# Kernel tuning notes

Hardware: AMD Instinct MI355X
Metric: run time of the kernel (lower is better)

Reference implementation:

```python
import jax, jax.numpy as jnp
import numpy as np

B, L, C, D, M = 64, 256, 8, 512, 512


def setup_inputs() -> dict:
    key = jax.random.key(0)
    ks = jax.random.split(key, 12)
    sd = 1.0 / np.sqrt(D)
    sm = 1.0 / np.sqrt(M)
    return {
        "x": jax.random.normal(ks[0], (B, L, D), jnp.float32),
        "x_c": jax.random.randint(ks[1], (B, L, C), 0, L),
        "x_m": jax.random.uniform(ks[2], (B, L), jnp.float32),
        "x_m_c": jax.random.uniform(ks[3], (B, L, C), jnp.float32),
        "W_ioux": jax.random.uniform(ks[4], (3 * M, D), jnp.float32, -sd, sd),
        "b_ioux": jax.random.uniform(ks[5], (3 * M,), jnp.float32, -sd, sd),
        "W_iouh": jax.random.uniform(ks[6], (3 * M, M), jnp.float32, -sm, sm),
        "b_iouh": jax.random.uniform(ks[7], (3 * M,), jnp.float32, -sm, sm),
        "W_fx": jax.random.uniform(ks[8], (M, D), jnp.float32, -sd, sd),
        "b_fx": jax.random.uniform(ks[9], (M,), jnp.float32, -sd, sd),
        "W_fh": jax.random.uniform(ks[10], (M, M), jnp.float32, -sm, sm),
        "b_fh": jax.random.uniform(ks[11], (M,), jnp.float32, -sm, sm),
    }


def reference(x, x_c, x_m, x_m_c, W_ioux, b_ioux, W_iouh, b_iouh, W_fx, b_fx, W_fh, b_fh):
    bsz, len_seq, in_dim = x.shape
    mem = W_fx.shape[0]
    outputs0 = jnp.zeros((bsz, len_seq, 2 * mem), x.dtype)  # row 0 = init_state = zeros
    prev0 = jnp.zeros((bsz, 2 * mem), x.dtype)
    # time-major streams for steps 1..L-1
    xs = (
        jnp.arange(1, len_seq),
        jnp.swapaxes(x, 0, 1)[1:],
        jnp.swapaxes(x_c, 0, 1)[1:],
        jnp.swapaxes(x_m, 0, 1)[1:],
        jnp.swapaxes(x_m_c, 0, 1)[1:],
    )

    def step(carry, inputs):
        outputs, prev = carry
        t, x_t, xc_t, xm_t, xmc_t = inputs
        # gather child states [B, C, 2M] from outputs buffer
        idx = jnp.broadcast_to(xc_t[:, :, None], (bsz, xc_t.shape[1], 2 * mem))
        child = jnp.take_along_axis(outputs, idx, axis=1)
        c_s, c_h = child[..., :mem], child[..., mem:]
        mc = xmc_t[..., None]  # [B, C, 1]
        child_h_sum = jnp.sum(c_h * mc, axis=1)  # [B, M]
        iou = x_t @ W_ioux.T + b_ioux + child_h_sum @ W_iouh.T + b_iouh
        i, o, u = jnp.split(iou, 3, axis=-1)
        i, o, u = jax.nn.sigmoid(i), jax.nn.sigmoid(o), jnp.tanh(u)
        f = jax.nn.sigmoid(c_h @ W_fh.T + b_fh + (x_t @ W_fx.T + b_fx)[:, None, :])
        c = i * u + jnp.sum(f * c_s * mc, axis=1)
        h = o * jnp.tanh(c)
        s = jnp.concatenate([c, h], axis=-1)
        m = xm_t[:, None]
        s = m * s + (1.0 - m) * prev
        outputs = jax.lax.dynamic_update_slice(outputs, s[:, None, :], (0, t, 0))
        return (outputs, s), None

    (outputs, final_state), _ = jax.lax.scan(step, (outputs0, prev0), xs)
    return outputs, final_state
```

## Files before the change

kernel.cpp:

```cpp
#include <hip/hip_runtime.h>
#include <math.h>

namespace {

constexpr int Bn = 64, Ln = 256, Cn = 8, Dn = 512, Mn = 512;
constexpr int TWO_M = 2 * Mn;
constexpr int PCOLS = 2048;
constexpr size_t P_FLOATS = (size_t)Bn * Ln * PCOLS;
constexpr size_t P_BYTES  = P_FLOATS * 4;

__device__ __forceinline__ float sigmoidf_(float v) { return 1.0f / (1.0f + __expf(-v)); }
__device__ __forceinline__ float dot4_(float4 a, float4 b) {
    return a.x * b.x + a.y * b.y + a.z * b.z + a.w * b.w;
}

constexpr int PJLD = 36;

__global__ __launch_bounds__(256)
void proj2_kernel(const float* __restrict__ x,
                  const float* __restrict__ W_ioux, const float* __restrict__ b_ioux,
                  const float* __restrict__ b_iouh,
                  const float* __restrict__ W_fx, const float* __restrict__ b_fx,
                  float* __restrict__ P)
{
    __shared__ float sA[64 * PJLD];
    __shared__ float sB[64 * PJLD];
    const int tid = threadIdx.x;
    const int rb = blockIdx.x >> 5;
    const int cb = blockIdx.x & 31;
    const int r0 = rb * 64, c0 = cb * 64;
    const bool is_iou = (c0 < 3 * Mn);
    const int ri = tid & 15, ci = tid >> 4;

    float acc[4][4];
    #pragma unroll
    for (int r = 0; r < 4; ++r)
        #pragma unroll
        for (int c = 0; c < 4; ++c) acc[r][c] = 0.f;

    for (int k0 = 0; k0 < Dn; k0 += 32) {
        #pragma unroll
        for (int i = 0; i < 2; ++i) {
            const int flat = i * 256 + tid;
            const int row = flat >> 3, kq = flat & 7;
            *(float4*)&sA[row * PJLD + kq * 4] =
                *(const float4*)&x[(size_t)(r0 + row) * Dn + k0 + kq * 4];
            const float* wsrc = is_iou ? &W_ioux[(size_t)(c0 + row) * Dn]
                                       : &W_fx[(size_t)(c0 - 3 * Mn + row) * Dn];
            *(float4*)&sB[row * PJLD + kq * 4] = *(const float4*)&wsrc[k0 + kq * 4];
        }
        __syncthreads();
        #pragma unroll
        for (int k4 = 0; k4 < 8; ++k4) {
            float4 av[4], bv[4];
            #pragma unroll
            for (int r = 0; r < 4; ++r) av[r] = *(const float4*)&sA[(ri + r * 16) * PJLD + k4 * 4];
            #pragma unroll
            for (int c = 0; c < 4; ++c) bv[c] = *(const float4*)&sB[(ci + c * 16) * PJLD + k4 * 4];
            #pragma unroll
            for (int r = 0; r < 4; ++r)
                #pragma unroll
                for (int c = 0; c < 4; ++c) acc[r][c] += dot4_(av[r], bv[c]);
        }
        __syncthreads();
    }
    #pragma unroll
    for (int c = 0; c < 4; ++c) {
        const int col = c0 + ci + c * 16;
        const float bias = is_iou ? (b_ioux[col] + b_iouh[col]) : b_fx[col - 3 * Mn];
        #pragma unroll
        for (int r = 0; r < 4; ++r)
            P[(size_t)(r0 + ri + r * 16) * PCOLS + col] = acc[r][c] + bias;
    }
}

constexpr int PW2 = 0;
constexpr int PW2_SZ = 16 * 16 * 9 * 4;
constexpr int PW1 = PW2 + PW2_SZ;
constexpr int PW1_SZ = 16 * 2 * 192 * 4;
constexpr int PHS = PW1 + PW1_SZ;
constexpr int PFD = PHS + 4096;
constexpr int PIO = PFD + 1024;
constexpr int PCS = PIO + 384;
constexpr int PPV = PCS + 1024;
constexpr int PXMC = PPV + 256;
constexpr int PXM = PXMC + 64;
constexpr int PXC = PXM + 8;
constexpr int P_LDS_FLOATS = PXC + 64;
constexpr size_t P_LDS_BYTES = (size_t)P_LDS_FLOATS * 4;
static_assert(P_LDS_BYTES <= 163840, "persist3 LDS over budget");

__global__ __launch_bounds__(512, 2)
void persist3_kernel(const int* __restrict__ x_c, const float* __restrict__ x_m,
                     const float* __restrict__ x_m_c,
                     const float* __restrict__ W_iouh, const float* __restrict__ W_fh,
                     const float* __restrict__ b_fh, const float* __restrict__ P,
                     float* __restrict__ out, unsigned* __restrict__ ctr)
{
    extern __shared__ float lds[];
    float* w2   = lds + PW2;
    float* w1   = lds + PW1;
    float* s_hs = lds + PHS;
    float* s_fd = lds + PFD;
    float* s_io = lds + PIO;
    float* s_cs = lds + PCS;
    float* s_pv = lds + PPV;
    float* s_xmc = lds + PXMC;
    float* s_xm  = lds + PXM;
    int*   s_xc  = (int*)(lds + PXC);

    const int tid = threadIdx.x;
    const int g  = blockIdx.x & 7;
    const int mt = blockIdx.x >> 3;
    const int m0 = mt * 16;
    const int b0 = g * 8;
    unsigned* myctr = ctr + g * 32;

    #pragma unroll
    for (int chk = 0; chk < 4; ++chk) {
        const int q = chk * 512 + tid;
        const int i = q >> 7, col = (q >> 3) & 15, ks = q & 7;
        *(float4*)&w2[(i * 144 + col * 9 + ks) * 4] =
            *(const float4*)&W_fh[(size_t)(m0 + col) * Dn + ks * 4 + i * 32];
    }
    #pragma unroll
    for (int chk = 0; chk < 12; ++chk) {
        const int q = chk * 512 + tid;
        const int i = q / 384, r1 = q % 384;
        const int cc = r1 / 192, m = r1 % 192;
        const int cq = m >> 3, ks = m & 7;
        const int c = cq * 2 + cc, s = c >> 4, j = c & 15;
        *(float4*)&w1[q * 4] =
            *(const float4*)&W_iouh[(size_t)(s * Mn + m0 + j) * Mn + ks * 4 + i * 32];
    }
    const float bfh_j = b_fh[m0 + (tid & 15)];
    if (tid < 256) s_pv[tid] = 0.f;

    const int g2_rq = tid >> 5, g2_jh = (tid >> 3) & 3, g2_ks = tid & 7;
    const int g1_bq = tid / 192, g1_r = tid % 192;
    const int g1_cq = g1_r >> 3, g1_ks = g1_r & 7;
    const int p1_b = tid >> 6, p1_k = tid & 63;
    __syncthreads();

    for (int t = 1; t < Ln; ++t) {
        float p0 = 0.f, p1 = 0.f, p2 = 0.f, p3 = 0.f;
        if (tid < 128) {
            const size_t prow = ((size_t)(b0 + (tid >> 4)) * Ln + t) * (size_t)PCOLS
                                + m0 + (tid & 15);
            p0 = P[prow];           p1 = P[prow + Mn];
            p2 = P[prow + 2 * Mn];  p3 = P[prow + 3 * Mn];
        }
        if (tid < 64) {
            const int b = tid >> 3, c = tid & 7;
            const int idx = x_c[((size_t)(b0 + b) * Ln + t) * Cn + c];
            s_xc[tid]  = (idx < t) ? idx : 0;
            s_xmc[tid] = x_m_c[((size_t)(b0 + b) * Ln + t) * Cn + c];
        } else if (tid < 72) {
            s_xm[tid - 64] = x_m[(size_t)(b0 + tid - 64) * Ln + t];
        }
        __syncthreads();

        {
            const float* rowp[8];
            float wt[8];
            #pragma unroll
            for (int c = 0; c < 8; ++c) {
                rowp[c] = &out[((size_t)(b0 + p1_b) * Ln + s_xc[p1_b * 8 + c]) * TWO_M + Mn];
                wt[c] = s_xmc[p1_b * 8 + c];
            }
            #pragma unroll
            for (int i = 0; i < 2; ++i) {
                const int k = p1_k * 4 + i * 256;
                float4 hs = make_float4(0.f, 0.f, 0.f, 0.f);
                #pragma unroll
                for (int c = 0; c < 8; ++c) {
                    const float4 v = *(const float4*)&rowp[c][k];
                    hs.x += wt[c] * v.x; hs.y += wt[c] * v.y;
                    hs.z += wt[c] * v.z; hs.w += wt[c] * v.w;
                }
                *(float4*)&s_hs[p1_b * 512 + k] = hs;
            }
        }
        if (tid < 256) {
            const int row = tid >> 2, q = tid & 3;
            const float4 v = *(const float4*)&out[((size_t)(b0 + (row >> 3)) * Ln
                                                   + s_xc[row]) * TWO_M + m0 + q * 4];
            *(float4*)&s_cs[row * 16 + q * 4] = v;
        }
        __syncthreads();

        {
            const float* rp[4];
            #pragma unroll
            for (int r = 0; r < 4; ++r) {
                const int row = g2_rq * 4 + r;
                rp[r] = &out[((size_t)(b0 + (row >> 3)) * Ln + s_xc[row]) * TWO_M + Mn];
            }
            float acc[4][4];
            #pragma unroll
            for (int r = 0; r < 4; ++r)
                #pragma unroll
                for (int jj = 0; jj < 4; ++jj) acc[r][jj] = 0.f;
            #pragma unroll 4
            for (int i = 0; i < 16; ++i) {
                const int k = g2_ks * 4 + i * 32;
                float4 cv[4], wv[4];
                #pragma unroll
                for (int r = 0; r < 4; ++r) cv[r] = *(const float4*)&rp[r][k];
                #pragma unroll
                for (int jj = 0; jj < 4; ++jj)
                    wv[jj] = *(const float4*)&w2[(i * 144 + (g2_jh * 4 + jj) * 9 + g2_ks) * 4];
                #pragma unroll
                for (int r = 0; r < 4; ++r)
                    #pragma unroll
                    for (int jj = 0; jj < 4; ++jj) acc[r][jj] += dot4_(cv[r], wv[jj]);
            }
            #pragma unroll
            for (int r = 0; r < 4; ++r)
                #pragma unroll
                for (int jj = 0; jj < 4; ++jj) {
                    float v = acc[r][jj];
                    v += __shfl_xor(v, 1); v += __shfl_xor(v, 2); v += __shfl_xor(v, 4);
                    acc[r][jj] = v;
                }
            if (g2_ks == 0) {
                #pragma unroll
                for (int r = 0; r < 4; ++r)
                    *(float4*)&s_fd[(g2_rq * 4 + r) * 16 + g2_jh * 4] =
                        make_float4(acc[r][0], acc[r][1], acc[r][2], acc[r][3]);
            }
        }
        if (tid < 384) {
            float acc[2][4];
            #pragma unroll
            for (int cc = 0; cc < 2; ++cc)
                #pragma unroll
                for (int bb = 0; bb < 4; ++bb) acc[cc][bb] = 0.f;
            #pragma unroll 4
            for (int i = 0; i < 16; ++i) {
                const int k = g1_ks * 4 + i * 32;
                float4 hv[4];
                #pragma unroll
                for (int bb = 0; bb < 4; ++bb)
                    hv[bb] = *(const float4*)&s_hs[(g1_bq * 4 + bb) * 512 + k];
                #pragma unroll
                for (int cc = 0; cc < 2; ++cc) {
                    const float4 wv = *(const float4*)&w1[((i * 2 + cc) * 192
                                                           + g1_cq * 8 + g1_ks) * 4];
                    #pragma unroll
                    for (int bb = 0; bb < 4; ++bb) acc[cc][bb] += dot4_(hv[bb], wv);
                }
            }
            #pragma unroll
            for (int cc = 0; cc < 2; ++cc)
                #pragma unroll
                for (int bb = 0; bb < 4; ++bb) {
                    float v = acc[cc][bb];
                    v += __shfl_xor(v, 1); v += __shfl_xor(v, 2); v += __shfl_xor(v, 4);
                    acc[cc][bb] = v;
                }
            if (g1_ks == 0) {
                #pragma unroll
                for (int cc = 0; cc < 2; ++cc)
                    #pragma unroll
                    for (int bb = 0; bb < 4; ++bb)
                        s_io[(g1_bq * 4 + bb) * 48 + g1_cq * 2 + cc] = acc[cc][bb];
            }
        }
        __syncthreads();

        if (tid < 128) {
            const int b = tid >> 4, j = tid & 15;
            const float iv = s_io[b * 48 + j]      + p0;
            const float ov = s_io[b * 48 + 16 + j] + p1;
            const float uv = s_io[b * 48 + 32 + j] + p2;
            const float i_ = sigmoidf_(iv);
            const float o_ = sigmoidf_(ov);
            const float u_ = tanhf(uv);
            float facc = 0.f;
            #pragma unroll
            for (int c = 0; c < 8; ++c) {
                const int row = b * 8 + c;
                const float f = sigmoidf_(s_fd[row * 16 + j] + bfh_j + p3);
                facc += f * s_cs[row * 16 + j] * s_xmc[row];
            }
            const float cv = i_ * u_ + facc;
            const float hv = o_ * tanhf(cv);
            const float mv = s_xm[b];
            const float nc = mv * cv + (1.f - mv) * s_pv[b * 32 + j];
            const float nh = mv * hv + (1.f - mv) * s_pv[b * 32 + 16 + j];
            const size_t ob = ((size_t)(b0 + b) * Ln + t) * TWO_M;
            out[ob + m0 + j]      = nc;
            out[ob + Mn + m0 + j] = nh;
            s_pv[b * 32 + j]      = nc;
            s_pv[b * 32 + 16 + j] = nh;
        }
        __syncthreads();

        if (t < Ln - 1) {
            if (tid == 0) {
                __hip_atomic_fetch_add(myctr, 1u, __ATOMIC_RELEASE, __HIP_MEMORY_SCOPE_AGENT);
                const unsigned target = 32u * (unsigned)t;
                while (__hip_atomic_load(myctr, __ATOMIC_RELAXED, __HIP_MEMORY_SCOPE_AGENT) < target)
                    __builtin_amdgcn_s_sleep(2);
                (void)__hip_atomic_load(myctr, __ATOMIC_ACQUIRE, __HIP_MEMORY_SCOPE_AGENT);
            }
            __syncthreads();
        }
    }
}

constexpr int LBT = 4, LMT = 32, LNMT = Mn / LMT, LPAD = 4, LDK = Dn + LPAD;
constexpr int L_U16 = 4096, L_CHS = LBT * LDK, L_CH = LBT * Cn * LDK,
              L_WFH = LMT * LDK, L_CS = LBT * Cn * LMT, L_IOUF = 4 * LBT * LMT;
constexpr int L_FLOATS = L_U16 + L_CHS + L_CH + L_WFH + L_CS + L_IOUF + 32 + 4 + 32;
constexpr size_t L_BYTES = (size_t)L_FLOATS * 4;

__global__ __launch_bounds__(256, 1)
void step_legacy(const float* __restrict__ x, const int* __restrict__ x_c,
                 const float* __restrict__ x_m, const float* __restrict__ x_m_c,
                 const float* __restrict__ W_ioux, const float* __restrict__ b_ioux,
                 const float* __restrict__ W_iouh, const float* __restrict__ b_iouh,
                 const float* __restrict__ W_fx, const float* __restrict__ b_fx,
                 const float* __restrict__ W_fh, const float* __restrict__ b_fh,
                 float* __restrict__ out, int t)
{
    extern __shared__ float lds[];
    float* u16    = lds;
    float* s_chs  = u16 + L_U16;
    float* s_ch   = s_chs + L_CHS;
    float* s_wfh  = s_ch + L_CH;
    float* s_cs   = s_wfh + L_WFH;
    float* s_iouf = s_cs + L_CS;
    float* s_xmc  = s_iouf + L_IOUF;
    float* s_xm   = s_xmc + 32;
    int*   s_xc   = (int*)(s_xm + 4);

    const int tid = threadIdx.x;
    const int mt = blockIdx.x & (LNMT - 1);
    const int bt = blockIdx.x >> 4;
    const int b0 = bt * LBT, m0 = mt * LMT;

    #pragma unroll
    for (int i = 0; i < 8; ++i) {
        int flat = i * 256 + tid, b = flat >> 9, k = flat & 511;
        u16[b * LDK + k] = x[((size_t)(b0 + b) * Ln + t) * Dn + k];
    }
    if (tid < 32) {
        int b = tid >> 3, c = tid & 7;
        s_xc[tid]  = x_c[((size_t)(b0 + b) * Ln + t) * Cn + c];
        s_xmc[tid] = x_m_c[((size_t)(b0 + b) * Ln + t) * Cn + c];
    }
    if (tid < 4) s_xm[tid] = x_m[(size_t)(b0 + tid) * Ln + t];
    for (int i = 0; i < 64; ++i) {
        int flat = i * 256 + tid, j = flat >> 9, k = flat & 511;
        s_wfh[j * LDK + k] = W_fh[(size_t)(m0 + j) * Dn + k];
    }
    __syncthreads();

    #pragma unroll
    for (int i = 0; i < 8; ++i) {
        int flat = i * 256 + tid, b = flat >> 9, k = flat & 511;
        float acc = 0.f;
        #pragma unroll
        for (int c = 0; c < 8; ++c) {
            int idx = s_xc[b * 8 + c];
            float v = 0.f;
            if (idx < t) v = out[((size_t)(b0 + b) * Ln + idx) * TWO_M + Mn + k];
            s_ch[(b * 8 + c) * LDK + k] = v;
            acc += s_xmc[b * 8 + c] * v;
        }
        s_chs[b * LDK + k] = acc;
    }
    #pragma unroll
    for (int i = 0; i < 4; ++i) {
        int flat = i * 256 + tid;
        int b = flat >> 8, rem = flat & 255, c = rem >> 5, j = rem & 31;
        int idx = s_xc[b * 8 + c];
        float v = 0.f;
        if (idx < t) v = out[((size_t)(b0 + b) * Ln + idx) * TWO_M + m0 + j];
        s_cs[flat] = v;
    }
    __syncthreads();

    {
        const int unit = tid >> 3, ksl = tid & 7, s = unit >> 3, jg = unit & 7;
        float acc[4][4];
        #pragma unroll
        for (int b = 0; b < 4; ++b)
            #pragma unroll
            for (int jj = 0; jj < 4; ++jj) acc[b][jj] = 0.f;
        if (s < 3) {
            const int colbase = s * Mn + m0 + jg * 4;
            #pragma unroll 4
            for (int it = 0; it < 16; ++it) {
                const int k = it * 32 + ksl * 4;
                float4 sx[4], sc[4];
                #pragma unroll
                for (int b = 0; b < 4; ++b) {
                    sx[b] = *(const float4*)&u16[b * LDK + k];
                    sc[b] = *(const float4*)&s_chs[b * LDK + k];
                }
                #pragma unroll
                for (int jj = 0; jj < 4; ++jj) {
                    const float4 wx = *(const float4*)&W_ioux[(size_t)(colbase + jj) * Dn + k];
                    const float4 wh = *(const float4*)&W_iouh[(size_t)(colbase + jj) * Dn + k];
                    #pragma unroll
                    for (int b = 0; b < 4; ++b)
                        acc[b][jj] += dot4_(sx[b], wx) + dot4_(sc[b], wh);
                }
            }
        } else {
            const int colbase = m0 + jg * 4;
            #pragma unroll 4
            for (int it = 0; it < 16; ++it) {
                const int k = it * 32 + ksl * 4;
                float4 sx[4];
                #pragma unroll
                for (int b = 0; b < 4; ++b) sx[b] = *(const float4*)&u16[b * LDK + k];
                #pragma unroll
                for (int jj = 0; jj < 4; ++jj) {
                    const float4 wx = *(const float4*)&W_fx[(size_t)(colbase + jj) * Dn + k];
                    #pragma unroll
                    for (int b = 0; b < 4; ++b) acc[b][jj] += dot4_(sx[b], wx);
                }
            }
        }
        __syncthreads();
        #pragma unroll
        for (int b = 0; b < 4; ++b)
            #pragma unroll
            for (int jj = 0; jj < 4; ++jj)
                u16[unit * 128 + ksl * 16 + b * 4 + jj] = acc[b][jj];
        __syncthreads();
        #pragma unroll
        for (int e = 0; e < 2; ++e) {
            const int task = e * 256 + tid;
            const int unit2 = task >> 4, rem = task & 15;
            float v = 0.f;
            #pragma unroll
            for (int k2 = 0; k2 < 8; ++k2) v += u16[unit2 * 128 + k2 * 16 + rem];
            const int s2 = unit2 >> 3, jg2 = unit2 & 7;
            const int bb = rem >> 2, jj = rem & 3, j = jg2 * 4 + jj;
            float bias = (s2 < 3) ? (b_ioux[s2 * Mn + m0 + j] + b_iouh[s2 * Mn + m0 + j])
                                  : b_fx[m0 + j];
            s_iouf[(s2 * 4 + bb) * 32 + j] = v + bias;
        }
    }
    __syncthreads();

    {
        const int pos = tid >> 2, ksc = tid & 3, rg = pos >> 3, jg = pos & 7;
        float acc[4][4];
        #pragma unroll
        for (int r = 0; r < 4; ++r)
            #pragma unroll
            for (int j = 0; j < 4; ++j) acc[r][j] = 0.f;
        #pragma unroll 4
        for (int it = 0; it < 32; ++it) {
            const int k = it * 16 + ksc * 4;
            float4 ch[4], wf[4];
            #pragma unroll
            for (int r = 0; r < 4; ++r) ch[r] = *(const float4*)&s_ch[(rg * 4 + r) * LDK + k];
            #pragma unroll
            for (int j = 0; j < 4; ++j) wf[j] = *(const float4*)&s_wfh[(jg * 4 + j) * LDK + k];
            #pragma unroll
            for (int r = 0; r < 4; ++r)
                #pragma unroll
                for (int j = 0; j < 4; ++j) acc[r][j] += dot4_(ch[r], wf[j]);
        }
        #pragma unroll
        for (int r = 0; r < 4; ++r)
            #pragma unroll
            for (int j = 0; j < 4; ++j)
                u16[((rg * 4 + r) * 32 + (jg * 4 + j)) * 4 + ksc] = acc[r][j];
    }
    __syncthreads();

    if (tid < 128) {
        const int b = tid >> 5, j = tid & 31;
        const float iv  = s_iouf[(0 * 4 + b) * 32 + j];
        const float ov  = s_iouf[(1 * 4 + b) * 32 + j];
        const float uv  = s_iouf[(2 * 4 + b) * 32 + j];
        const float fxv = s_iouf[(3 * 4 + b) * 32 + j];
        const float i_ = sigmoidf_(iv), o_ = sigmoidf_(ov), u_ = tanhf(uv);
        const float bfh = b_fh[m0 + j];
        float facc = 0.f;
        #pragma unroll
        for (int c = 0; c < 8; ++c) {
            const int row = b * 8 + c;
            const float fd = u16[(row * 32 + j) * 4 + 0] + u16[(row * 32 + j) * 4 + 1]
                           + u16[(row * 32 + j) * 4 + 2] + u16[(row * 32 + j) * 4 + 3];
            const float f = sigmoidf_(fd + bfh + fxv);
            facc += f * s_cs[row * 32 + j] * s_xmc[row];
        }
        const float cval = i_ * u_ + facc;
        const float hval = o_ * tanhf(cval);
        const float mval = s_xm[b];
        const size_t base  = ((size_t)(b0 + b) * Ln + t) * TWO_M;
        const size_t pbase = ((size_t)(b0 + b) * Ln + (t - 1)) * TWO_M;
        out[base + m0 + j]      = mval * cval + (1.f - mval) * out[pbase + m0 + j];
        out[base + Mn + m0 + j] = mval * hval + (1.f - mval) * out[pbase + Mn + m0 + j];
    }
}

__global__ void zero_row0(float* __restrict__ out) {
    int i = blockIdx.x * 256 + threadIdx.x;
    int b = i >> 10, j = i & 1023;
    out[(size_t)b * Ln * TWO_M + j] = 0.f;
}

__global__ void zero_ctr(unsigned* __restrict__ c) {
    if (threadIdx.x < 8) c[threadIdx.x * 32] = 0u;
}

__global__ void final_copy(const float* __restrict__ out, float* __restrict__ fin) {
    int i = blockIdx.x * 256 + threadIdx.x;
    int b = i >> 10, j = i & 1023;
    fin[i] = out[((size_t)b * Ln + (Ln - 1)) * TWO_M + j];
}

}

extern "C" void kernel_launch(void* const* d_in, const int* in_sizes, int n_in,
                              void* d_out, int out_size, void* d_ws, size_t ws_size,
                              hipStream_t stream) {
    (void)in_sizes; (void)n_in; (void)out_size;
    const float* x      = (const float*)d_in[0];
    const int*   x_c    = (const int*)d_in[1];
    const float* x_m    = (const float*)d_in[2];
    const float* x_m_c  = (const float*)d_in[3];
    const float* W_ioux = (const float*)d_in[4];
    const float* b_ioux = (const float*)d_in[5];
    const float* W_iouh = (const float*)d_in[6];
    const float* b_iouh = (const float*)d_in[7];
    const float* W_fx   = (const float*)d_in[8];
    const float* b_fx   = (const float*)d_in[9];
    const float* W_fh   = (const float*)d_in[10];
    const float* b_fh   = (const float*)d_in[11];
    float* out = (float*)d_out;
    float* fin = out + (size_t)Bn * Ln * TWO_M;

    hipFuncSetAttribute((const void*)persist3_kernel,
                        hipFuncAttributeMaxDynamicSharedMemorySize, (int)P_LDS_BYTES);
    hipFuncSetAttribute((const void*)step_legacy,
                        hipFuncAttributeMaxDynamicSharedMemorySize, (int)L_BYTES);

    hipLaunchKernelGGL(zero_row0, dim3(256), dim3(256), 0, stream, out);

    if (ws_size >= P_BYTES) {
        float* Pp = (float*)d_ws;
        unsigned* ctr = (unsigned*)d_ws;
        hipLaunchKernelGGL(proj2_kernel, dim3(8192), dim3(256), 0, stream,
                           x, W_ioux, b_ioux, b_iouh, W_fx, b_fx, Pp);
        hipLaunchKernelGGL(zero_ctr, dim3(1), dim3(64), 0, stream, ctr);
        void* kargs[] = { (void*)&x_c, (void*)&x_m, (void*)&x_m_c, (void*)&W_iouh,
                          (void*)&W_fh, (void*)&b_fh, (void*)&Pp, (void*)&out,
                          (void*)&ctr };
        hipLaunchCooperativeKernel((const void*)persist3_kernel, dim3(256), dim3(512),
                                   kargs, (unsigned)P_LDS_BYTES, stream);
    } else {
        for (int t = 1; t < Ln; ++t) {
            hipLaunchKernelGGL(step_legacy, dim3(256), dim3(256), L_BYTES, stream,
                               x, x_c, x_m, x_m_c, W_ioux, b_ioux, W_iouh, b_iouh,
                               W_fx, b_fx, W_fh, b_fh, out, t);
        }
    }
    hipLaunchKernelGGL(final_copy, dim3(256), dim3(256), 0, stream, out, fin);
}
```

Measured before the change: 5.130 ms.

## Keep W_fh slice in registers, prefetch next-step inputs, precompute child row offsets

```diff
diff --git a/kernel.cpp b/kernel.cpp
--- a/kernel.cpp
+++ b/kernel.cpp
@@ -74,40 +74,38 @@
     }
 }
 
-constexpr int PW2 = 0;
-constexpr int PW2_SZ = 16 * 16 * 9 * 4;
-constexpr int PW1 = PW2 + PW2_SZ;
-constexpr int PW1_SZ = 16 * 2 * 192 * 4;
-constexpr int PHS = PW1 + PW1_SZ;
-constexpr int PFD = PHS + 4096;
-constexpr int PIO = PFD + 1024;
-constexpr int PCS = PIO + 384;
-constexpr int PPV = PCS + 1024;
-constexpr int PXMC = PPV + 256;
-constexpr int PXM = PXMC + 64;
-constexpr int PXC = PXM + 8;
-constexpr int P_LDS_FLOATS = PXC + 64;
-constexpr size_t P_LDS_BYTES = (size_t)P_LDS_FLOATS * 4;
-static_assert(P_LDS_BYTES <= 163840, "persist3 LDS over budget");
-
-__global__ __launch_bounds__(512, 2)
-void persist3_kernel(const int* __restrict__ x_c, const float* __restrict__ x_m,
+constexpr int Q_W1  = 0;
+constexpr int Q_HS  = Q_W1 + 24576;
+constexpr int Q_FD  = Q_HS + 4096;
+constexpr int Q_IO  = Q_FD + 1024;
+constexpr int Q_CS  = Q_IO + 384;
+constexpr int Q_PV  = Q_CS + 1024;
+constexpr int Q_XMC = Q_PV + 256;
+constexpr int Q_XM  = Q_XMC + 64;
+constexpr int Q_XC  = Q_XM + 8;
+constexpr int Q_RB  = Q_XC + 64;
+constexpr int Q_FLOATS = Q_RB + 64;
+constexpr size_t Q_LDS_BYTES = (size_t)Q_FLOATS * 4;
+static_assert(Q_LDS_BYTES <= 163840, "persist4 LDS over budget");
+
+__global__ __launch_bounds__(512, 1)
+void persist4_kernel(const int* __restrict__ x_c, const float* __restrict__ x_m,
                      const float* __restrict__ x_m_c,
                      const float* __restrict__ W_iouh, const float* __restrict__ W_fh,
                      const float* __restrict__ b_fh, const float* __restrict__ P,
                      float* __restrict__ out, unsigned* __restrict__ ctr)
 {
     extern __shared__ float lds[];
-    float* w2   = lds + PW2;
-    float* w1   = lds + PW1;
-    float* s_hs = lds + PHS;
-    float* s_fd = lds + PFD;
-    float* s_io = lds + PIO;
-    float* s_cs = lds + PCS;
-    float* s_pv = lds + PPV;
-    float* s_xmc = lds + PXMC;
-    float* s_xm  = lds + PXM;
-    int*   s_xc  = (int*)(lds + PXC);
+    float* w1    = lds + Q_W1;
+    float* s_hs  = lds + Q_HS;
+    float* s_fd  = lds + Q_FD;
+    float* s_io  = lds + Q_IO;
+    float* s_cs  = lds + Q_CS;
+    float* s_pv  = lds + Q_PV;
+    float* s_xmc = lds + Q_XMC;
+    float* s_xm  = lds + Q_XM;
+    int*   s_xc  = (int*)(lds + Q_XC);
+    int*   s_rb  = (int*)(lds + Q_RB);
 
     const int tid = threadIdx.x;
     const int g  = blockIdx.x & 7;
@@ -116,13 +114,6 @@
     const int b0 = g * 8;
     unsigned* myctr = ctr + g * 32;
 
-    #pragma unroll
-    for (int chk = 0; chk < 4; ++chk) {
-        const int q = chk * 512 + tid;
-        const int i = q >> 7, col = (q >> 3) & 15, ks = q & 7;
-        *(float4*)&w2[(i * 144 + col * 9 + ks) * 4] =
-            *(const float4*)&W_fh[(size_t)(m0 + col) * Dn + ks * 4 + i * 32];
-    }
     #pragma unroll
     for (int chk = 0; chk < 12; ++chk) {
         const int q = chk * 512 + tid;
@@ -133,30 +124,48 @@
         *(float4*)&w1[q * 4] =
             *(const float4*)&W_iouh[(size_t)(s * Mn + m0 + j) * Mn + ks * 4 + i * 32];
     }
-    const float bfh_j = b_fh[m0 + (tid & 15)];
-    if (tid < 256) s_pv[tid] = 0.f;
-
-    const int g2_rq = tid >> 5, g2_jh = (tid >> 3) & 3, g2_ks = tid & 7;
+
+    const int g2_ks = tid & 15, g2_jh = (tid >> 4) & 7, g2_rq = tid >> 7;
+    float4 w2r[2][8];
+    #pragma unroll
+    for (int cc = 0; cc < 2; ++cc)
+        #pragma unroll
+        for (int i = 0; i < 8; ++i)
+            w2r[cc][i] = *(const float4*)&W_fh[(size_t)(m0 + g2_jh * 2 + cc) * Dn
+                                               + g2_ks * 4 + i * 64];
+
     const int g1_bq = tid / 192, g1_r = tid % 192;
     const int g1_cq = g1_r >> 3, g1_ks = g1_r & 7;
     const int p1_b = tid >> 6, p1_k = tid & 63;
+
+    const float bfh_j = b_fh[m0 + (tid & 15)];
+    if (tid < 256) s_pv[tid] = 0.f;
+
+    int   sc_idx = 0;  float sc_xmc = 0.f, sc_xm = 0.f;
+    float p0 = 0.f, p1 = 0.f, p2 = 0.f, p3 = 0.f;
+    if (tid < 64) {
+        const int b = tid >> 3, c = tid & 7;
+        sc_idx = x_c[((size_t)(b0 + b) * Ln + 1) * Cn + c];
+        sc_xmc = x_m_c[((size_t)(b0 + b) * Ln + 1) * Cn + c];
+    } else if (tid < 72) {
+        sc_xm = x_m[(size_t)(b0 + tid - 64) * Ln + 1];
+    }
+    if (tid < 128) {
+        const size_t prow = ((size_t)(b0 + (tid >> 4)) * Ln + 1) * (size_t)PCOLS
+                            + m0 + (tid & 15);
+        p0 = P[prow];           p1 = P[prow + Mn];
+        p2 = P[prow + 2 * Mn];  p3 = P[prow + 3 * Mn];
+    }
     __syncthreads();
 
     for (int t = 1; t < Ln; ++t) {
-        float p0 = 0.f, p1 = 0.f, p2 = 0.f, p3 = 0.f;
-        if (tid < 128) {
-            const size_t prow = ((size_t)(b0 + (tid >> 4)) * Ln + t) * (size_t)PCOLS
-                                + m0 + (tid & 15);
-            p0 = P[prow];           p1 = P[prow + Mn];
-            p2 = P[prow + 2 * Mn];  p3 = P[prow + 3 * Mn];
-        }
         if (tid < 64) {
-            const int b = tid >> 3, c = tid & 7;
-            const int idx = x_c[((size_t)(b0 + b) * Ln + t) * Cn + c];
-            s_xc[tid]  = (idx < t) ? idx : 0;
-            s_xmc[tid] = x_m_c[((size_t)(b0 + b) * Ln + t) * Cn + c];
+            const int ci = (sc_idx < t) ? sc_idx : 0;
+            s_xc[tid]  = ci;
+            s_xmc[tid] = sc_xmc;
+            s_rb[tid]  = ((b0 + (tid >> 3)) * Ln + ci) * TWO_M;
         } else if (tid < 72) {
-            s_xm[tid - 64] = x_m[(size_t)(b0 + tid - 64) * Ln + t];
+            s_xm[tid - 64] = sc_xm;
         }
         __syncthreads();
 
@@ -165,7 +174,7 @@
             float wt[8];
             #pragma unroll
             for (int c = 0; c < 8; ++c) {
-                rowp[c] = &out[((size_t)(b0 + p1_b) * Ln + s_xc[p1_b * 8 + c]) * TWO_M + Mn];
+                rowp[c] = &out[(size_t)s_rb[p1_b * 8 + c] + Mn];
                 wt[c] = s_xmc[p1_b * 8 + c];
             }
             #pragma unroll
@@ -183,51 +192,49 @@
         }
         if (tid < 256) {
             const int row = tid >> 2, q = tid & 3;
-            const float4 v = *(const float4*)&out[((size_t)(b0 + (row >> 3)) * Ln
-                                                   + s_xc[row]) * TWO_M + m0 + q * 4];
+            const float4 v = *(const float4*)&out[(size_t)s_rb[row] + m0 + q * 4];
             *(float4*)&s_cs[row * 16 + q * 4] = v;
         }
         __syncthreads();
 
         {
-            const float* rp[4];
-            #pragma unroll
-            for (int r = 0; r < 4; ++r) {
-                const int row = g2_rq * 4 + r;
-                rp[r] = &out[((size_t)(b0 + (row >> 3)) * Ln + s_xc[row]) * TWO_M + Mn];
-            }
-            float acc[4][4];
-            #pragma unroll
-            for (int r = 0; r < 4; ++r)
-                #pragma unroll
-                for (int jj = 0; jj < 4; ++jj) acc[r][jj] = 0.f;
-            #pragma unroll 4
-            for (int i = 0; i < 16; ++i) {
-                const int k = g2_ks * 4 + i * 32;
-                float4 cv[4], wv[4];
-                #pragma unroll
-                for (int r = 0; r < 4; ++r) cv[r] = *(const float4*)&rp[r][k];
-                #pragma unroll
-                for (int jj = 0; jj < 4; ++jj)
-                    wv[jj] = *(const float4*)&w2[(i * 144 + (g2_jh * 4 + jj) * 9 + g2_ks) * 4];
-                #pragma unroll
-                for (int r = 0; r < 4; ++r)
+            int rb[16];
+            #pragma unroll
+            for (int rr = 0; rr < 16; ++rr) rb[rr] = s_rb[g2_rq * 16 + rr];
+            float acc2[16][2];
+            #pragma unroll
+            for (int rr = 0; rr < 16; ++rr) { acc2[rr][0] = 0.f; acc2[rr][1] = 0.f; }
+            #pragma unroll 2
+            for (int i = 0; i < 8; ++i) {
+                const int k4 = Mn + g2_ks * 4 + i * 64;
+                #pragma unroll
+                for (int h = 0; h < 2; ++h) {
+                    float4 cv[8];
                     #pragma unroll
-                    for (int jj = 0; jj < 4; ++jj) acc[r][jj] += dot4_(cv[r], wv[jj]);
-            }
-            #pragma unroll
-            for (int r = 0; r < 4; ++r)
-                #pragma unroll
-                for (int jj = 0; jj < 4; ++jj) {
-                    float v = acc[r][jj];
-                    v += __shfl_xor(v, 1); v += __shfl_xor(v, 2); v += __shfl_xor(v, 4);
-                    acc[r][jj] = v;
+                    for (int r2 = 0; r2 < 8; ++r2)
+                        cv[r2] = *(const float4*)&out[(size_t)rb[h * 8 + r2] + k4];
+                    #pragma unroll
+                    for (int r2 = 0; r2 < 8; ++r2) {
+                        acc2[h * 8 + r2][0] += dot4_(cv[r2], w2r[0][i]);
+                        acc2[h * 8 + r2][1] += dot4_(cv[r2], w2r[1][i]);
+                    }
+                }
+            }
+            #pragma unroll
+            for (int rr = 0; rr < 16; ++rr)
+                #pragma unroll
+                for (int cc = 0; cc < 2; ++cc) {
+                    float v = acc2[rr][cc];
+                    v += __shfl_xor(v, 1); v += __shfl_xor(v, 2);
+                    v += __shfl_xor(v, 4); v += __shfl_xor(v, 8);
+                    acc2[rr][cc] = v;
                 }
             if (g2_ks == 0) {
                 #pragma unroll
-                for (int r = 0; r < 4; ++r)
-                    *(float4*)&s_fd[(g2_rq * 4 + r) * 16 + g2_jh * 4] =
-                        make_float4(acc[r][0], acc[r][1], acc[r][2], acc[r][3]);
+                for (int rr = 0; rr < 16; ++rr) {
+                    s_fd[(g2_rq * 16 + rr) * 16 + g2_jh * 2]     = acc2[rr][0];
+                    s_fd[(g2_rq * 16 + rr) * 16 + g2_jh * 2 + 1] = acc2[rr][1];
+                }
             }
         }
         if (tid < 384) {
@@ -265,6 +272,25 @@
                     #pragma unroll
                     for (int bb = 0; bb < 4; ++bb)
                         s_io[(g1_bq * 4 + bb) * 48 + g1_cq * 2 + cc] = acc[cc][bb];
+            }
+        }
+
+        int   nx_idx = 0;  float nx_xmc = 0.f, nx_xm = 0.f;
+        float np0 = 0.f, np1 = 0.f, np2 = 0.f, np3 = 0.f;
+        if (t < Ln - 1) {
+            const int tn = t + 1;
+            if (tid < 64) {
+                const int b = tid >> 3, c = tid & 7;
+                nx_idx = x_c[((size_t)(b0 + b) * Ln + tn) * Cn + c];
+                nx_xmc = x_m_c[((size_t)(b0 + b) * Ln + tn) * Cn + c];
+            } else if (tid < 72) {
+                nx_xm = x_m[(size_t)(b0 + tid - 64) * Ln + tn];
+            }
+            if (tid < 128) {
+                const size_t prow = ((size_t)(b0 + (tid >> 4)) * Ln + tn) * (size_t)PCOLS
+                                    + m0 + (tid & 15);
+                np0 = P[prow];           np1 = P[prow + Mn];
+                np2 = P[prow + 2 * Mn];  np3 = P[prow + 3 * Mn];
             }
         }
         __syncthreads();
@@ -307,6 +333,8 @@
             }
             __syncthreads();
         }
+        sc_idx = nx_idx; sc_xmc = nx_xmc; sc_xm = nx_xm;
+        p0 = np0; p1 = np1; p2 = np2; p3 = np3;
     }
 }
 
@@ -541,8 +569,8 @@
     float* out = (float*)d_out;
     float* fin = out + (size_t)Bn * Ln * TWO_M;
 
-    hipFuncSetAttribute((const void*)persist3_kernel,
-                        hipFuncAttributeMaxDynamicSharedMemorySize, (int)P_LDS_BYTES);
+    hipFuncSetAttribute((const void*)persist4_kernel,
+                        hipFuncAttributeMaxDynamicSharedMemorySize, (int)Q_LDS_BYTES);
     hipFuncSetAttribute((const void*)step_legacy,
                         hipFuncAttributeMaxDynamicSharedMemorySize, (int)L_BYTES);
 
@@ -557,8 +585,8 @@
         void* kargs[] = { (void*)&x_c, (void*)&x_m, (void*)&x_m_c, (void*)&W_iouh,
                           (void*)&W_fh, (void*)&b_fh, (void*)&Pp, (void*)&out,
                           (void*)&ctr };
-        hipLaunchCooperativeKernel((const void*)persist3_kernel, dim3(256), dim3(512),
-                                   kargs, (unsigned)P_LDS_BYTES, stream);
+        hipLaunchCooperativeKernel((const void*)persist4_kernel, dim3(256), dim3(512),
+                                   kargs, (unsigned)Q_LDS_BYTES, stream);
     } else {
         for (int t = 1; t < Ln; ++t) {
             hipLaunchKernelGGL(step_legacy, dim3(256), dim3(256), L_BYTES, stream,
```

Result: slower. 7.091 ms (+38.2%).
